# Kernel tuning notes

Measured on AMD Instinct MI355X. Metric: run time of the kernel, lower is better.

## Reference

```python
import jax, jax.numpy as jnp
import numpy as np

B, L, D, H, FFN = 4, 2048, 1024, 8, 2048
DH = D // H  # 128

def layer_norm(x, g, b, eps=1e-5):
    m = jnp.mean(x, axis=-1, keepdims=True)
    v = jnp.mean((x - m) ** 2, axis=-1, keepdims=True)
    return (x - m) * jax.lax.rsqrt(v + eps) * g + b

def setup_inputs() -> dict:
    key = jax.random.key(0)
    ks = jax.random.split(key, 12)
    s = 0.02
    return {
        "inputs": jax.random.normal(ks[0], (B, L, D), jnp.float32),
        "Wq": jax.random.normal(ks[1], (D, D), jnp.float32) * s,
        "bq": jnp.zeros((D,), jnp.float32),
        "Wk": jax.random.normal(ks[2], (D, D), jnp.float32) * s,
        "bk": jnp.zeros((D,), jnp.float32),
        "Wv": jax.random.normal(ks[3], (D, D), jnp.float32) * s,
        "bv": jnp.zeros((D,), jnp.float32),
        "Wo": jax.random.normal(ks[4], (D, D), jnp.float32) * s,
        "bo": jnp.zeros((D,), jnp.float32),
        "ln1_g": jnp.ones((D,), jnp.float32),
        "ln1_b": jnp.zeros((D,), jnp.float32),
        "W1": jax.random.normal(ks[5], (FFN, D), jnp.float32) * s,
        "b1": jnp.zeros((FFN,), jnp.float32),
        "W2": jax.random.normal(ks[6], (D, FFN), jnp.float32) * s,
        "b2": jnp.zeros((D,), jnp.float32),
        "ln2_g": jnp.ones((D,), jnp.float32),
        "ln2_b": jnp.zeros((D,), jnp.float32),
    }

def reference(inputs, Wq, bq, Wk, bk, Wv, bv, Wo, bo, ln1_g, ln1_b, W1, b1, W2, b2, ln2_g, ln2_b):
    b, l, d = inputs.shape
    # linear projections then the original's raw row-major view (no head transpose)
    q = (inputs @ Wq.T + bq).reshape(b * H, -1, DH)
    k = (inputs @ Wk.T + bk).reshape(b * H, -1, DH)
    v = (inputs @ Wv.T + bv).reshape(b * H, -1, DH)
    scale = DH ** -0.5  # (2 * (d_k//2))^-0.5 in the original
    atten = jax.nn.softmax(jnp.einsum('bqd,bkd->bqk', q, k) * scale, axis=-1)
    context = jnp.einsum('bqk,bkd->bqd', atten, v).reshape(b, -1, H * DH)
    out = context @ Wo.T + bo
    h = layer_norm(inputs + out, ln1_g, ln1_b)  # residual + LN (dropout=0)
    # PositionwiseFeedForward: 1x1 conv1d == per-token linear
    f = jax.nn.relu(h @ W1.T + b1) @ W2.T + b2
    y = layer_norm(h + f, ln2_g, ln2_b)
    return (y, atten)
```

## Files before the change

kernel.cpp:

```cpp
#include <hip/hip_runtime.h>
#include <stdint.h>

using f32x4  = __attribute__((ext_vector_type(4))) float;
using f32x16 = __attribute__((ext_vector_type(16))) float;
using bf16x8 = __attribute__((ext_vector_type(8))) short;

#define DEV static __device__ __forceinline__

DEV unsigned short f2bf(float f){
  union { float f; unsigned int u; } c; c.f = f;
  unsigned int u = c.u;
  u += 0x7FFFu + ((u >> 16) & 1u);
  return (unsigned short)(u >> 16);
}
DEV float bf2f(unsigned short u){
  union { unsigned int u; float f; } c; c.u = ((unsigned int)u) << 16; return c.f;
}

DEV void gld_lds16(const void* g, void* l){
  __builtin_amdgcn_global_load_lds(
      (const __attribute__((address_space(1))) void*)g,
      (__attribute__((address_space(3))) void*)l, 16, 0, 0);
}

struct CvtArgs { const float* src[7]; int cum[8]; };
__global__ __launch_bounds__(256) void cvt_multi(CvtArgs a, unsigned short* __restrict__ dst){
  const int total = a.cum[7];
  for (int i = (blockIdx.x*256 + threadIdx.x)*4; i < total; i += gridDim.x*1024){
    int s = 0;
    #pragma unroll
    for (int k = 1; k < 7; ++k) s += (i >= a.cum[k]);
    const float* src = a.src[s];
    const int off = i - a.cum[s];
    float4 v = *(const float4*)(src + off);
    ushort4 o; o.x=f2bf(v.x); o.y=f2bf(v.y); o.z=f2bf(v.z); o.w=f2bf(v.w);
    *(ushort4*)(dst + i) = o;
  }
}

template<bool OUT_BF16, bool RELU, bool HAS_BIAS>
__global__ __launch_bounds__(512, 2)
void gemm_bt2(const unsigned short* __restrict__ Ap, const unsigned short* __restrict__ Bp,
              const float* __restrict__ bias, void* __restrict__ Cp, int N, int K)
{
  __shared__ __align__(16) char lds[131072];
  const int tid  = threadIdx.x;
  const int lane = tid & 63;
  const int wid  = tid >> 6;
  const int wm   = wid >> 2;
  const int wn   = wid & 3;
  const int mrow = lane & 15;
  const int krow = lane >> 4;

  const int nbx = N >> 7;
  const int nwg = gridDim.x;
  const int d   = blockIdx.x;
  const int swz = (d & 7)*(nwg >> 3) + (d >> 3);
  const int bx  = swz % nbx, by = swz / nbx;

  const size_t Kb = (size_t)K * 2;
  const char* Ab = (const char*)(Ap + (size_t)by*256*K);
  const char* Bb = (const char*)(Bp + (size_t)bx*128*K);
  const int NT = K >> 6;

  auto stageA = [&](int t){
    char* dst = lds + (t % 3)*32768;
    const char* src = Ab + (size_t)t*128;
    #pragma unroll
    for (int s = 0; s < 4; ++s){
      int o = s*8192 + tid*16;
      int row = o >> 7, cb = o & 127;
      gld_lds16(src + (size_t)row*Kb + (cb ^ ((row & 7) << 4)), dst + o);
    }
  };
  auto stageB = [&](int t){
    char* dst = lds + 98304 + (t & 1)*16384;
    const char* src = Bb + (size_t)t*128;
    #pragma unroll
    for (int s = 0; s < 2; ++s){
      int o = s*8192 + tid*16;
      int row = o >> 7, cb = o & 127;
      gld_lds16(src + (size_t)row*Kb + (cb ^ ((row & 7) << 4)), dst + o);
    }
  };

  f32x4 acc[8][2] = {};

  stageA(0); stageB(0); stageA(1);
  asm volatile("s_waitcnt vmcnt(4)" ::: "memory");
  __builtin_amdgcn_s_barrier();

  for (int t = 0; t < NT; ++t){
    if (t + 1 < NT) stageB(t + 1);
    if (t + 2 < NT) stageA(t + 2);

    const char* baseA = lds + (t % 3)*32768;
    const char* baseB = lds + 98304 + (t & 1)*16384;

    bf16x8 b[2][2];
    #pragma unroll
    for (int ni = 0; ni < 2; ++ni){
      int row = wn*32 + ni*16 + mrow;
      #pragma unroll
      for (int ks = 0; ks < 2; ++ks)
        b[ni][ks] = *(const bf16x8*)(baseB + row*128 + ((ks*64 + krow*16) ^ ((row & 7) << 4)));
    }
    bf16x8 a[8][2];
    #pragma unroll
    for (int mi = 0; mi < 8; ++mi){
      int row = wm*128 + mi*16 + mrow;
      #pragma unroll
      for (int ks = 0; ks < 2; ++ks)
        a[mi][ks] = *(const bf16x8*)(baseA + row*128 + ((ks*64 + krow*16) ^ ((row & 7) << 4)));
    }

    __builtin_amdgcn_s_setprio(1);
    #pragma unroll
    for (int ks = 0; ks < 2; ++ks)
      #pragma unroll
      for (int mi = 0; mi < 8; ++mi)
        #pragma unroll
        for (int ni = 0; ni < 2; ++ni)
          acc[mi][ni] = __builtin_amdgcn_mfma_f32_16x16x32_bf16(a[mi][ks], b[ni][ks], acc[mi][ni], 0, 0, 0);
    __builtin_amdgcn_s_setprio(0);

    if (t + 1 < NT){
      if (t + 2 < NT) asm volatile("s_waitcnt vmcnt(4)" ::: "memory");
      else            asm volatile("s_waitcnt vmcnt(0)" ::: "memory");
      __builtin_amdgcn_s_barrier();
      __builtin_amdgcn_sched_barrier(0);
    }
  }

  int row0 = by*256 + wm*128;
  int col0 = bx*128 + wn*32;
  #pragma unroll
  for (int mi = 0; mi < 8; ++mi){
    #pragma unroll
    for (int ni = 0; ni < 2; ++ni){
      int col = col0 + ni*16 + mrow;
      float bv = HAS_BIAS ? bias[col] : 0.f;
      #pragma unroll
      for (int r = 0; r < 4; ++r){
        int row = row0 + mi*16 + krow*4 + r;
        float v = acc[mi][ni][r] + bv;
        if (RELU) v = fmaxf(v, 0.f);
        if (OUT_BF16) ((unsigned short*)Cp)[(size_t)row*N + col] = f2bf(v);
        else          ((float*)Cp)[(size_t)row*N + col] = v;
      }
    }
  }
}

__global__ __launch_bounds__(512, 2)
void gemm_qkv(const unsigned short* __restrict__ Ap, const unsigned short* __restrict__ Bp,
              const float* __restrict__ bq, const float* __restrict__ bk,
              const float* __restrict__ bv,
              unsigned short* __restrict__ Qo, unsigned short* __restrict__ Ko,
              unsigned short* __restrict__ Vto)
{
  constexpr int N = 3072, K = 1024;
  __shared__ __align__(16) char lds[131072];
  const int tid  = threadIdx.x;
  const int lane = tid & 63;
  const int wid  = tid >> 6;
  const int wm   = wid >> 2;
  const int wn   = wid & 3;
  const int mrow = lane & 15;
  const int krow = lane >> 4;

  const int nbx = N >> 7;
  const int nwg = gridDim.x;
  const int d   = blockIdx.x;
  const int swz = (d & 7)*(nwg >> 3) + (d >> 3);
  const int bx  = swz % nbx, by = swz / nbx;

  const size_t Kb = (size_t)K * 2;
  const char* Ab = (const char*)(Ap + (size_t)by*256*K);
  const char* Bb = (const char*)(Bp + (size_t)bx*128*K);
  const int NT = K >> 6;

  auto stageA = [&](int t){
    char* dst = lds + (t % 3)*32768;
    const char* src = Ab + (size_t)t*128;
    #pragma unroll
    for (int s = 0; s < 4; ++s){
      int o = s*8192 + tid*16;
      int row = o >> 7, cb = o & 127;
      gld_lds16(src + (size_t)row*Kb + (cb ^ ((row & 7) << 4)), dst + o);
    }
  };
  auto stageB = [&](int t){
    char* dst = lds + 98304 + (t & 1)*16384;
    const char* src = Bb + (size_t)t*128;
    #pragma unroll
    for (int s = 0; s < 2; ++s){
      int o = s*8192 + tid*16;
      int row = o >> 7, cb = o & 127;
      gld_lds16(src + (size_t)row*Kb + (cb ^ ((row & 7) << 4)), dst + o);
    }
  };

  f32x4 acc[8][2] = {};

  stageA(0); stageB(0); stageA(1);
  asm volatile("s_waitcnt vmcnt(4)" ::: "memory");
  __builtin_amdgcn_s_barrier();

  for (int t = 0; t < NT; ++t){
    if (t + 1 < NT) stageB(t + 1);
    if (t + 2 < NT) stageA(t + 2);

    const char* baseA = lds + (t % 3)*32768;
    const char* baseB = lds + 98304 + (t & 1)*16384;

    bf16x8 b[2][2];
    #pragma unroll
    for (int ni = 0; ni < 2; ++ni){
      int row = wn*32 + ni*16 + mrow;
      #pragma unroll
      for (int ks = 0; ks < 2; ++ks)
        b[ni][ks] = *(const bf16x8*)(baseB + row*128 + ((ks*64 + krow*16) ^ ((row & 7) << 4)));
    }
    bf16x8 a[8][2];
    #pragma unroll
    for (int mi = 0; mi < 8; ++mi){
      int row = wm*128 + mi*16 + mrow;
      #pragma unroll
      for (int ks = 0; ks < 2; ++ks)
        a[mi][ks] = *(const bf16x8*)(baseA + row*128 + ((ks*64 + krow*16) ^ ((row & 7) << 4)));
    }

    __builtin_amdgcn_s_setprio(1);
    #pragma unroll
    for (int ks = 0; ks < 2; ++ks)
      #pragma unroll
      for (int mi = 0; mi < 8; ++mi)
        #pragma unroll
        for (int ni = 0; ni < 2; ++ni)
          acc[mi][ni] = __builtin_amdgcn_mfma_f32_16x16x32_bf16(a[mi][ks], b[ni][ks], acc[mi][ni], 0, 0, 0);
    __builtin_amdgcn_s_setprio(0);

    if (t + 1 < NT){
      if (t + 2 < NT) asm volatile("s_waitcnt vmcnt(4)" ::: "memory");
      else            asm volatile("s_waitcnt vmcnt(0)" ::: "memory");
      __builtin_amdgcn_s_barrier();
      __builtin_amdgcn_sched_barrier(0);
    }
  }

  const int row0  = by*256 + wm*128;
  const int col0g = bx*128 + wn*32;
  const int which = col0g >> 10;
  const float* bias = which == 0 ? bq : (which == 1 ? bk : bv);
  unsigned short* out01 = which == 0 ? Qo : Ko;

  if (which < 2){
    #pragma unroll
    for (int mi = 0; mi < 8; ++mi){
      #pragma unroll
      for (int ni = 0; ni < 2; ++ni){
        int cq = (col0g & 1023) + ni*16 + mrow;
        float bvv = bias[cq];
        #pragma unroll
        for (int r = 0; r < 4; ++r){
          int row = row0 + mi*16 + krow*4 + r;
          out01[(size_t)row*1024 + cq] = f2bf(acc[mi][ni][r] + bvv);
        }
      }
    }
  } else {
    #pragma unroll
    for (int mi = 0; mi < 8; ++mi){
      #pragma unroll
      for (int ni = 0; ni < 2; ++ni){
        int cq = (col0g & 1023) + ni*16 + mrow;
        float bvv = bias[cq];
        int rowb = row0 + mi*16 + krow*4;
        int gg = rowb >> 11;
        int j  = rowb & 2047;
        ushort4 o;
        o.x = f2bf(acc[mi][ni][0] + bvv);
        o.y = f2bf(acc[mi][ni][1] + bvv);
        o.z = f2bf(acc[mi][ni][2] + bvv);
        o.w = f2bf(acc[mi][ni][3] + bvv);
        *(ushort4*)(Vto + (size_t)gg*262144 + (size_t)cq*2048 + j) = o;
      }
    }
  }
}

__global__ __launch_bounds__(256, 2) void attn_fused(
    const unsigned short* __restrict__ Q, const unsigned short* __restrict__ K,
    const unsigned short* __restrict__ Vt, float* __restrict__ P,
    unsigned short* __restrict__ CTX)
{
  __shared__ __align__(16) char lds[65536];
  char* ldsK = lds;
  char* ldsV = lds + 32768;
  const int tid  = threadIdx.x;
  const int lane = tid & 63;
  const int w    = tid >> 6;
  const int l31  = lane & 31;
  const int hi   = lane >> 5;
  const float scale = 0.08838834764831845f;

  const int d  = blockIdx.x;
  const int i  = d >> 3;
  const int g  = (d & 7) + 8*(i >> 4);
  const int q0 = (i & 15) * 128;

  const char* KbB = (const char*)(K  + (size_t)g*262144);
  const char* VtB = (const char*)(Vt + (size_t)g*262144);
  const unsigned short* Qb = Q + (size_t)g*262144 + (size_t)(q0 + w*32)*128;
  float* Pb = P + (size_t)g*4194304 + (size_t)(q0 + w*32)*2048;

  bf16x8 qf[8];
  #pragma unroll
  for (int kk = 0; kk < 8; ++kk)
    qf[kk] = *(const bf16x8*)((const char*)Qb + (size_t)l31*256 + kk*32 + hi*16);

  auto stageK = [&](int buf, int j0b){
    #pragma unroll
    for (int r = 0; r < 4; ++r){
      int o = r*4096 + tid*16;
      int j = o >> 8, c = o & 255;
      gld_lds16(KbB + (size_t)(j0b + j)*256 + (c ^ ((j & 15) << 4)),
                ldsK + buf*16384 + o);
    }
  };
  auto stageV = [&](int buf, int j0b){
    #pragma unroll
    for (int r = 0; r < 4; ++r){
      int o = r*4096 + tid*16;
      int e = o >> 7, c = o & 127;
      gld_lds16(VtB + (size_t)e*4096 + j0b*2 + (c ^ ((e & 7) << 4)),
                ldsV + buf*16384 + o);
    }
  };
  auto readK = [&](int buf, int jloc, int kk) -> bf16x8 {
    int row = jloc + l31;
    int col = (kk*32 + hi*16) ^ ((l31 & 15) << 4);
    return *(const bf16x8*)(ldsK + buf*16384 + row*256 + col);
  };
  auto readV = [&](int buf, int jloc, int c16, int t) -> bf16x8 {
    int row = t*32 + l31;
    int col = (jloc*2 + c16*32 + hi*16) ^ ((row & 7) << 4);
    return *(const bf16x8*)(ldsV + buf*16384 + row*128 + col);
  };

  int buf = 0;
  stageK(0, 0);
  __syncthreads();
  float lacc = 0.f;
  for (int st = 0; st < 32; ++st){
    if (st < 31) stageK(buf ^ 1, (st + 1) * 64);
    #pragma unroll
    for (int jt = 0; jt < 2; ++jt){
      const int jloc = jt * 32;
      f32x16 s1 = {}, s2 = {};
      #pragma unroll
      for (int kk = 0; kk < 4; ++kk){
        s1 = __builtin_amdgcn_mfma_f32_32x32x16_bf16(readK(buf, jloc, kk),   qf[kk],   s1, 0, 0, 0);
        s2 = __builtin_amdgcn_mfma_f32_32x32x16_bf16(readK(buf, jloc, kk+4), qf[kk+4], s2, 0, 0, 0);
      }
      #pragma unroll
      for (int r = 0; r < 16; ++r) lacc += __expf((s1[r] + s2[r]) * scale);
    }
    __syncthreads();
    buf ^= 1;
  }
  lacc += __shfl_xor(lacc, 32, 64);
  const float invl = 1.f / lacc;

  stageK(0, 0); stageV(0, 0);
  __syncthreads();
  f32x16 O[4] = {};
  buf = 0;
  for (int st = 0; st < 32; ++st){
    if (st < 31){ stageK(buf ^ 1, (st + 1) * 64); stageV(buf ^ 1, (st + 1) * 64); }
    #pragma unroll
    for (int jt = 0; jt < 2; ++jt){
      const int jloc  = jt * 32;
      const int jglob = st*64 + jloc;
      f32x16 s1 = {}, s2 = {};
      #pragma unroll
      for (int kk = 0; kk < 4; ++kk){
        s1 = __builtin_amdgcn_mfma_f32_32x32x16_bf16(readK(buf, jloc, kk),   qf[kk],   s1, 0, 0, 0);
        s2 = __builtin_amdgcn_mfma_f32_32x32x16_bf16(readK(buf, jloc, kk+4), qf[kk+4], s2, 0, 0, 0);
      }
      float p[16];
      #pragma unroll
      for (int r = 0; r < 16; ++r) p[r] = __expf((s1[r] + s2[r]) * scale) * invl;
      float* prow = Pb + (size_t)l31*2048 + jglob + hi*4;
      *(float4*)(prow)      = make_float4(p[0],  p[1],  p[2],  p[3]);
      *(float4*)(prow + 8)  = make_float4(p[4],  p[5],  p[6],  p[7]);
      *(float4*)(prow + 16) = make_float4(p[8],  p[9],  p[10], p[11]);
      *(float4*)(prow + 24) = make_float4(p[12], p[13], p[14], p[15]);
      unsigned int pk[8];
      #pragma unroll
      for (int ii = 0; ii < 8; ++ii)
        pk[ii] = (unsigned int)f2bf(p[2*ii]) | ((unsigned int)f2bf(p[2*ii+1]) << 16);
      unsigned int r0 = (unsigned int)__shfl_xor((int)(hi ? pk[0] : pk[2]), 32, 64);
      unsigned int r1 = (unsigned int)__shfl_xor((int)(hi ? pk[1] : pk[3]), 32, 64);
      unsigned int r2 = (unsigned int)__shfl_xor((int)(hi ? pk[4] : pk[6]), 32, 64);
      unsigned int r3 = (unsigned int)__shfl_xor((int)(hi ? pk[5] : pk[7]), 32, 64);
      union U { unsigned int u[4]; bf16x8 v; };
      U a0, a1;
      a0.u[0] = hi ? r0    : pk[0];  a0.u[1] = hi ? r1    : pk[1];
      a0.u[2] = hi ? pk[2] : r0;     a0.u[3] = hi ? pk[3] : r1;
      a1.u[0] = hi ? r2    : pk[4];  a1.u[1] = hi ? r3    : pk[5];
      a1.u[2] = hi ? pk[6] : r2;     a1.u[3] = hi ? pk[7] : r3;
      #pragma unroll
      for (int t = 0; t < 4; ++t){
        O[t] = __builtin_amdgcn_mfma_f32_32x32x16_bf16(a0.v, readV(buf, jloc, 0, t), O[t], 0, 0, 0);
        O[t] = __builtin_amdgcn_mfma_f32_32x32x16_bf16(a1.v, readV(buf, jloc, 1, t), O[t], 0, 0, 0);
      }
    }
    __syncthreads();
    buf ^= 1;
  }

  #pragma unroll
  for (int t = 0; t < 4; ++t){
    #pragma unroll
    for (int r = 0; r < 16; ++r){
      int qrow = (r & 3) + 8*(r >> 2) + 4*hi;
      CTX[(size_t)g*262144 + (size_t)(q0 + w*32 + qrow)*128 + t*32 + l31] = f2bf(O[t][r]);
    }
  }
}

DEV float block_sum256(float v, float* red){
  #pragma unroll
  for (int off = 32; off > 0; off >>= 1) v += __shfl_xor(v, off, 64);
  int lane = threadIdx.x & 63, wid = threadIdx.x >> 6;
  if (lane == 0) red[wid] = v;
  __syncthreads();
  return (red[0]+red[1]) + (red[2]+red[3]);
}

template<bool WRITE_F32, bool WRITE_BF>
__global__ __launch_bounds__(256) void ln_residual_bf(
    const unsigned short* __restrict__ A, const unsigned short* __restrict__ R,
    const float* __restrict__ gamma, const float* __restrict__ beta,
    float* __restrict__ outf, unsigned short* __restrict__ outb){
  __shared__ float red1[4], red2[4];
  long base = (long)blockIdx.x * 1024;
  int tid = threadIdx.x;
  ushort4 a = *(const ushort4*)(A + base + tid*4);
  ushort4 r = *(const ushort4*)(R + base + tid*4);
  float v[4] = { bf2f(a.x)+bf2f(r.x), bf2f(a.y)+bf2f(r.y),
                 bf2f(a.z)+bf2f(r.z), bf2f(a.w)+bf2f(r.w) };
  float s = (v[0]+v[1]) + (v[2]+v[3]);
  s = block_sum256(s, red1);
  float mean = s * (1.f/1024.f);
  float dd[4] = {v[0]-mean, v[1]-mean, v[2]-mean, v[3]-mean};
  float sq = (dd[0]*dd[0]+dd[1]*dd[1]) + (dd[2]*dd[2]+dd[3]*dd[3]);
  sq = block_sum256(sq, red2);
  float rstd = rsqrtf(sq*(1.f/1024.f) + 1e-5f);
  float4 g4 = *(const float4*)(gamma + tid*4);
  float4 b4 = *(const float4*)(beta  + tid*4);
  float o[4] = { dd[0]*rstd*g4.x + b4.x, dd[1]*rstd*g4.y + b4.y,
                 dd[2]*rstd*g4.z + b4.z, dd[3]*rstd*g4.w + b4.w };
  if (WRITE_F32){
    float4 o4; o4.x=o[0]; o4.y=o[1]; o4.z=o[2]; o4.w=o[3];
    *(float4*)(outf + base + tid*4) = o4;
  }
  if (WRITE_BF){
    ushort4 ob; ob.x=f2bf(o[0]); ob.y=f2bf(o[1]); ob.z=f2bf(o[2]); ob.w=f2bf(o[3]);
    *(ushort4*)(outb + base + tid*4) = ob;
  }
}

extern "C" void kernel_launch(void* const* d_in, const int* in_sizes, int n_in,
                              void* d_out, int out_size, void* d_ws, size_t ws_size,
                              hipStream_t stream){
  const float* X   = (const float*)d_in[0];
  const float* Wq  = (const float*)d_in[1];
  const float* bq  = (const float*)d_in[2];
  const float* Wk  = (const float*)d_in[3];
  const float* bk  = (const float*)d_in[4];
  const float* Wv  = (const float*)d_in[5];
  const float* bv  = (const float*)d_in[6];
  const float* Wo  = (const float*)d_in[7];
  const float* bo  = (const float*)d_in[8];
  const float* g1  = (const float*)d_in[9];
  const float* b1n = (const float*)d_in[10];
  const float* W1  = (const float*)d_in[11];
  const float* b1  = (const float*)d_in[12];
  const float* W2  = (const float*)d_in[13];
  const float* b2  = (const float*)d_in[14];
  const float* g2  = (const float*)d_in[15];
  const float* b2n = (const float*)d_in[16];

  const int M = 8192, D = 1024, F = 2048;
  const long YSZ = (long)M * D;
  float* y_out = (float*)d_out;
  float* atten = (float*)d_out + YSZ;

  char* w = (char*)d_ws;
  auto alloc = [&](size_t bytes){ char* p = w; w += (bytes + 255) & ~(size_t)255; return p; };
  unsigned short* Xbf   = (unsigned short*)alloc((size_t)M*D*2);
  unsigned short* Wqbf  = (unsigned short*)alloc((size_t)D*D*2);
  unsigned short* Wkbf  = (unsigned short*)alloc((size_t)D*D*2);
  unsigned short* Wvbf  = (unsigned short*)alloc((size_t)D*D*2);
  unsigned short* Wobf  = (unsigned short*)alloc((size_t)D*D*2);
  unsigned short* W1bf  = (unsigned short*)alloc((size_t)F*D*2);
  unsigned short* W2bf  = (unsigned short*)alloc((size_t)D*F*2);
  unsigned short* Qbf   = (unsigned short*)alloc((size_t)M*D*2);
  unsigned short* Kbf   = (unsigned short*)alloc((size_t)M*D*2);
  unsigned short* Vtbf  = (unsigned short*)alloc((size_t)M*D*2);
  unsigned short* CTXbf = (unsigned short*)alloc((size_t)M*D*2);
  unsigned short* Hbf   = (unsigned short*)alloc((size_t)M*D*2);
  unsigned short* F1bf  = (unsigned short*)alloc((size_t)M*F*2);
  unsigned short* TMPbf = (unsigned short*)alloc((size_t)M*D*2);
  (void)Wqbf; (void)Wkbf; (void)Wvbf;

  {
    CvtArgs a;
    a.src[0]=X; a.src[1]=Wq; a.src[2]=Wk; a.src[3]=Wv; a.src[4]=Wo; a.src[5]=W1; a.src[6]=W2;
    int MD = M*D, DD = D*D, FD = F*D;
    a.cum[0]=0;
    a.cum[1]=a.cum[0]+MD;  a.cum[2]=a.cum[1]+DD;  a.cum[3]=a.cum[2]+DD;
    a.cum[4]=a.cum[3]+DD;  a.cum[5]=a.cum[4]+DD;  a.cum[6]=a.cum[5]+FD;
    a.cum[7]=a.cum[6]+FD;
    cvt_multi<<<2048, 256, 0, stream>>>(a, Xbf);
  }

  dim3 blk2(512);

  gemm_qkv<<<dim3((M/256)*(3072/128)), blk2, 0, stream>>>(Xbf, Wqbf, bq, bk, bv, Qbf, Kbf, Vtbf);

  attn_fused<<<dim3(512), dim3(256), 0, stream>>>(Qbf, Kbf, Vtbf, atten, CTXbf);

  gemm_bt2<true,false,true><<<dim3((M/256)*(D/128)), blk2, 0, stream>>>(CTXbf, Wobf, bo, TMPbf, D, D);

  ln_residual_bf<false,true><<<M, 256, 0, stream>>>(Xbf, TMPbf, g1, b1n, nullptr, Hbf);

  gemm_bt2<true,true,true><<<dim3((M/256)*(F/128)), blk2, 0, stream>>>(Hbf, W1bf, b1, F1bf, F, D);

  gemm_bt2<true,false,true><<<dim3((M/256)*(D/128)), blk2, 0, stream>>>(F1bf, W2bf, b2, TMPbf, D, F);

  ln_residual_bf<true,false><<<M, 256, 0, stream>>>(Hbf, TMPbf, g2, b2n, y_out, nullptr);
}
```

Before: 440.6 us.

## Split attention softmax-denominator pass into separate split-K kernel

Moves the first pass of the attention kernel, which computes softmax row sums, into its own kernel. That kernel splits the key dimension into four chunks across 2048 blocks with higher occupancy and writes partial sums to a workspace buffer. The second kernel reads the four partials and does the probability write and PV pass as before. The aim is better GPU occupancy for the row-sum pass, which previously ran on only 512 blocks, at the cost of an extra launch and a small workspace round trip.

```diff
diff --git a/kernel.cpp b/kernel.cpp
--- a/kernel.cpp
+++ b/kernel.cpp
@@ -290,10 +290,82 @@
   }
 }
 
-__global__ __launch_bounds__(256, 2) void attn_fused(
+__global__ __launch_bounds__(256, 4) void attn_pass1(
     const unsigned short* __restrict__ Q, const unsigned short* __restrict__ K,
-    const unsigned short* __restrict__ Vt, float* __restrict__ P,
-    unsigned short* __restrict__ CTX)
+    float* __restrict__ Lp)
+{
+  __shared__ __align__(16) char lds[32768];
+  char* ldsK = lds;
+  const int tid  = threadIdx.x;
+  const int lane = tid & 63;
+  const int w    = tid >> 6;
+  const int l31  = lane & 31;
+  const int hi   = lane >> 5;
+  const float scale = 0.08838834764831845f;
+
+  const int d    = blockIdx.x;
+  const int g8   = d & 7;
+  const int rest = d >> 3;
+  const int qt   = rest & 15;
+  const int jq   = (rest >> 4) & 3;
+  const int gh   = rest >> 6;
+  const int g    = g8 + 8*gh;
+  const int q0   = qt * 128;
+  const int jbase = jq * 512;
+
+  const char* KbB = (const char*)(K + (size_t)g*262144);
+  const unsigned short* Qb = Q + (size_t)g*262144 + (size_t)(q0 + w*32)*128;
+
+  bf16x8 qf[8];
+  #pragma unroll
+  for (int kk = 0; kk < 8; ++kk)
+    qf[kk] = *(const bf16x8*)((const char*)Qb + (size_t)l31*256 + kk*32 + hi*16);
+
+  auto stageK = [&](int buf, int j0b){
+    #pragma unroll
+    for (int r = 0; r < 4; ++r){
+      int o = r*4096 + tid*16;
+      int j = o >> 8, c = o & 255;
+      gld_lds16(KbB + (size_t)(j0b + j)*256 + (c ^ ((j & 15) << 4)),
+                ldsK + buf*16384 + o);
+    }
+  };
+  auto readK = [&](int buf, int jloc, int kk) -> bf16x8 {
+    int row = jloc + l31;
+    int col = (kk*32 + hi*16) ^ ((l31 & 15) << 4);
+    return *(const bf16x8*)(ldsK + buf*16384 + row*256 + col);
+  };
+
+  int buf = 0;
+  stageK(0, jbase);
+  __syncthreads();
+  float lacc = 0.f;
+  for (int st = 0; st < 8; ++st){
+    if (st < 7) stageK(buf ^ 1, jbase + (st + 1) * 64);
+    #pragma unroll
+    for (int jt = 0; jt < 2; ++jt){
+      const int jloc = jt * 32;
+      f32x16 s1 = {}, s2 = {};
+      #pragma unroll
+      for (int kk = 0; kk < 4; ++kk){
+        s1 = __builtin_amdgcn_mfma_f32_32x32x16_bf16(readK(buf, jloc, kk),   qf[kk],   s1, 0, 0, 0);
+        s2 = __builtin_amdgcn_mfma_f32_32x32x16_bf16(readK(buf, jloc, kk+4), qf[kk+4], s2, 0, 0, 0);
+      }
+      #pragma unroll
+      for (int r = 0; r < 16; ++r) lacc += __expf((s1[r] + s2[r]) * scale);
+    }
+    __syncthreads();
+    buf ^= 1;
+  }
+  lacc += __shfl_xor(lacc, 32, 64);
+  if (hi == 0)
+    Lp[((size_t)g*2048 + q0 + w*32 + l31)*4 + jq] = lacc;
+}
+
+__global__ __launch_bounds__(256, 2) void attn_pass2(
+    const unsigned short* __restrict__ Q, const unsigned short* __restrict__ K,
+    const unsigned short* __restrict__ Vt, const float* __restrict__ Lp,
+    float* __restrict__ P, unsigned short* __restrict__ CTX)
 {
   __shared__ __align__(16) char lds[65536];
   char* ldsK = lds;
@@ -320,6 +392,9 @@
   for (int kk = 0; kk < 8; ++kk)
     qf[kk] = *(const bf16x8*)((const char*)Qb + (size_t)l31*256 + kk*32 + hi*16);
 
+  float4 lp = *(const float4*)(Lp + ((size_t)g*2048 + q0 + w*32 + l31)*4);
+  const float invl = 1.f / ((lp.x + lp.y) + (lp.z + lp.w));
+
   auto stageK = [&](int buf, int j0b){
     #pragma unroll
     for (int r = 0; r < 4; ++r){
@@ -350,33 +425,9 @@
   };
 
   int buf = 0;
-  stageK(0, 0);
-  __syncthreads();
-  float lacc = 0.f;
-  for (int st = 0; st < 32; ++st){
-    if (st < 31) stageK(buf ^ 1, (st + 1) * 64);
-    #pragma unroll
-    for (int jt = 0; jt < 2; ++jt){
-      const int jloc = jt * 32;
-      f32x16 s1 = {}, s2 = {};
-      #pragma unroll
-      for (int kk = 0; kk < 4; ++kk){
-        s1 = __builtin_amdgcn_mfma_f32_32x32x16_bf16(readK(buf, jloc, kk),   qf[kk],   s1, 0, 0, 0);
-        s2 = __builtin_amdgcn_mfma_f32_32x32x16_bf16(readK(buf, jloc, kk+4), qf[kk+4], s2, 0, 0, 0);
-      }
-      #pragma unroll
-      for (int r = 0; r < 16; ++r) lacc += __expf((s1[r] + s2[r]) * scale);
-    }
-    __syncthreads();
-    buf ^= 1;
-  }
-  lacc += __shfl_xor(lacc, 32, 64);
-  const float invl = 1.f / lacc;
-
   stageK(0, 0); stageV(0, 0);
   __syncthreads();
   f32x16 O[4] = {};
-  buf = 0;
   for (int st = 0; st < 32; ++st){
     if (st < 31){ stageK(buf ^ 1, (st + 1) * 64); stageV(buf ^ 1, (st + 1) * 64); }
     #pragma unroll
@@ -515,6 +566,7 @@
   unsigned short* Hbf   = (unsigned short*)alloc((size_t)M*D*2);
   unsigned short* F1bf  = (unsigned short*)alloc((size_t)M*F*2);
   unsigned short* TMPbf = (unsigned short*)alloc((size_t)M*D*2);
+  float*          Lp    = (float*)alloc((size_t)65536*4*4);
   (void)Wqbf; (void)Wkbf; (void)Wvbf;
 
   {
@@ -532,7 +584,9 @@
 
   gemm_qkv<<<dim3((M/256)*(3072/128)), blk2, 0, stream>>>(Xbf, Wqbf, bq, bk, bv, Qbf, Kbf, Vtbf);
 
-  attn_fused<<<dim3(512), dim3(256), 0, stream>>>(Qbf, Kbf, Vtbf, atten, CTXbf);
+  attn_pass1<<<dim3(2048), dim3(256), 0, stream>>>(Qbf, Kbf, Lp);
+
+  attn_pass2<<<dim3(512), dim3(256), 0, stream>>>(Qbf, Kbf, Vtbf, Lp, atten, CTXbf);
 
   gemm_bt2<true,false,true><<<dim3((M/256)*(D/128)), blk2, 0, stream>>>(CTXbf, Wobf, bo, TMPbf, D, D);
 
```

New measurement: 454.5 us. +3.2%, slower.
